# Kernel tuning notes

Hardware: AMD Instinct MI355X
Metric: run time of the kernel (lower is better)

The kernel has to match this reference:

```python
import jax, jax.numpy as jnp
import numpy as np

B, S, D = 2, 2048, 768
H = 12
HD = D // H


def setup_inputs() -> dict:
    key = jax.random.key(0)
    ks = jax.random.split(key, 9)
    s_in = 1.0 / np.sqrt(D)
    return {
        "x": jax.random.normal(ks[0], (B, S, D), dtype=jnp.float32),
        "wq": jax.random.normal(ks[1], (D, D), dtype=jnp.float32) * s_in,
        "bq": jax.random.normal(ks[2], (D,), dtype=jnp.float32) * 0.01,
        "wk": jax.random.normal(ks[3], (D, D), dtype=jnp.float32) * s_in,
        "bk": jax.random.normal(ks[4], (D,), dtype=jnp.float32) * 0.01,
        "wv": jax.random.normal(ks[5], (D, D), dtype=jnp.float32) * s_in,
        "bv": jax.random.normal(ks[6], (D,), dtype=jnp.float32) * 0.01,
        "wo": jax.random.normal(ks[7], (D, D), dtype=jnp.float32) * s_in,
        "bo": jax.random.normal(ks[8], (D,), dtype=jnp.float32) * 0.01,
    }


def reference(x, wq, bq, wk, bk, wv, bv, wo, bo):
    b, s, _ = x.shape
    # projections -> [b, h, s, hd]
    def proj(w, bias):
        return (x @ w + bias).reshape(b, s, H, HD).transpose(0, 2, 1, 3)
    q = proj(wq, bq)
    k = proj(wk, bk)
    v = proj(wv, bv)
    scores = jnp.einsum("bhqd,bhkd->bhqk", q, k)
    causal = jnp.triu(jnp.ones((s, s), dtype=bool), k=1)
    scores = jnp.where(causal, -jnp.inf, scores)
    attn = jax.nn.softmax(scores / np.sqrt(HD), axis=-1)
    # dropout p=0.0 -> identity
    ctx = jnp.einsum("bhqk,bhkd->bhqd", attn, v)
    ctx = ctx.transpose(0, 2, 1, 3).reshape(b, s, D)
    return ctx @ wo + bo
```

## Files before the change

kernel.cpp:

```cpp
#include <hip/hip_runtime.h>
#include <math.h>

#define BB  2
#define SS  2048
#define DD  768
#define HH  12
#define HDD 64
#define BSR (BB * SS)
#define NQT (SS / 64)
#define NCH 80
#define NKT 12

typedef __attribute__((ext_vector_type(8))) short bf16x8;
typedef __attribute__((ext_vector_type(4))) float f32x4;
typedef __attribute__((ext_vector_type(4))) int  i32x4;

__device__ inline f32x4 mfma16(bf16x8 a, bf16x8 b, f32x4 c) {
    return __builtin_amdgcn_mfma_f32_16x16x32_bf16(a, b, c, 0, 0, 0);
}

__device__ inline unsigned short f2b(float f) {
    unsigned int u = __float_as_uint(f);
    u += 0x7FFFu + ((u >> 16) & 1u);
    return (unsigned short)(u >> 16);
}
__device__ inline float b2f(unsigned short u) {
    return __uint_as_float((unsigned int)u << 16);
}

__device__ inline unsigned int cvt_pk_bf16(float lo, float hi) {
    unsigned int r;
    asm("v_cvt_pk_bf16_f32 %0, %1, %2" : "=v"(r) : "v"(lo), "v"(hi));
    return r;
}

__device__ inline void async_copy16(void* lds, const void* g) {
    __builtin_amdgcn_global_load_lds(
        (const __attribute__((address_space(1))) unsigned int*)g,
        (__attribute__((address_space(3))) unsigned int*)lds, 16, 0, 0);
}

__global__ __launch_bounds__(256) void conv_wT_kernel(
    const float* __restrict__ w0, const float* __restrict__ w1,
    const float* __restrict__ w2, const float* __restrict__ w3,
    unsigned short* __restrict__ o0, unsigned short* __restrict__ o1,
    unsigned short* __restrict__ o2, unsigned short* __restrict__ o3)
{
    const float* w = (blockIdx.z == 0) ? w0 : (blockIdx.z == 1) ? w1
                   : (blockIdx.z == 2) ? w2 : w3;
    unsigned short* o = (blockIdx.z == 0) ? o0 : (blockIdx.z == 1) ? o1
                      : (blockIdx.z == 2) ? o2 : o3;
    const int n0 = blockIdx.x * 64;
    const int k0 = blockIdx.y * 64;
    const int tid = threadIdx.x;

    __shared__ unsigned short tile[64][72];

#pragma unroll
    for (int p = 0; p < 4; ++p) {
        int c  = p * 256 + tid;
        int kr = c >> 4;
        int nc = (c & 15) * 4;
        float4 v = *(const float4*)&w[(size_t)(k0 + kr) * DD + n0 + nc];
        tile[nc + 0][kr] = f2b(v.x);
        tile[nc + 1][kr] = f2b(v.y);
        tile[nc + 2][kr] = f2b(v.z);
        tile[nc + 3][kr] = f2b(v.w);
    }
    __syncthreads();
#pragma unroll
    for (int p = 0; p < 2; ++p) {
        int c  = p * 256 + tid;
        int nr = c >> 3;
        int kc = (c & 7) * 8;
        *(i32x4*)&o[(size_t)(n0 + nr) * DD + k0 + kc] = *(const i32x4*)&tile[nr][kc];
    }
}

__global__ __launch_bounds__(256) void qkv_gemm_kernel(
    const float* __restrict__ x,
    const unsigned short* __restrict__ wqT, const unsigned short* __restrict__ wkT,
    const unsigned short* __restrict__ wvT,
    const float* __restrict__ bq, const float* __restrict__ bk,
    const float* __restrict__ bv,
    unsigned short* __restrict__ Qg, unsigned short* __restrict__ Kg,
    unsigned short* __restrict__ Vg)
{
    const int which = blockIdx.z;
    const unsigned short* Bt = (which == 0) ? wqT : (which == 1) ? wkT : wvT;
    const float* bias        = (which == 0) ? bq  : (which == 1) ? bk  : bv;
    unsigned short* out      = (which == 0) ? Qg  : (which == 1) ? Kg  : Vg;
    const float qs           = (which == 0) ? 0.18033688011112042f : 1.0f;

    const int m0 = blockIdx.x * 64;
    const int n0 = blockIdx.y * 128;
    const int tid  = threadIdx.x;
    const int w    = tid >> 6;
    const int lane = tid & 63;
    const int quad = lane >> 4;
    const int l16  = lane & 15;
    const int mh   = w & 1;
    const int nh   = w >> 1;
    const int swz  = l16 & 7;

    __shared__ unsigned short smem[24576];
    unsigned short (*As0)[64] = (unsigned short(*)[64])smem;
    unsigned short (*Bs0)[64] = (unsigned short(*)[64])(smem + 4096);
    unsigned short (*As1)[64] = (unsigned short(*)[64])(smem + 12288);
    unsigned short (*Bs1)[64] = (unsigned short(*)[64])(smem + 16384);
    unsigned short (*T)[136]  = (unsigned short(*)[136])smem;

    const int rA0 = tid >> 3,          jA0 = tid & 7,          chA0 = jA0 ^ (rA0 & 7);
    const int rA1 = (256 + tid) >> 3,  jA1 = tid & 7,          chA1 = jA1 ^ (rA1 & 7);
    const float* xr0 = &x[(size_t)(m0 + rA0) * DD + chA0 * 8];
    const float* xr1 = &x[(size_t)(m0 + rA1) * DD + chA1 * 8];
    int ldsA0 = rA0 * 64 + jA0 * 8;
    int ldsA1 = rA1 * 64 + jA1 * 8;

    const unsigned short* gB[4];
    int ldsB[4];
#pragma unroll
    for (int p = 0; p < 4; ++p) {
        int c  = p * 256 + tid;
        int r  = c >> 3;
        int j  = c & 7;
        int ch = j ^ (r & 7);
        gB[p]   = &Bt[(size_t)(n0 + r) * DD + ch * 8];
        ldsB[p] = r * 64 + j * 8;
    }

    f32x4 zero = {0.f, 0.f, 0.f, 0.f};
    f32x4 acc[2][4];
#pragma unroll
    for (int i = 0; i < 2; ++i)
#pragma unroll
        for (int j = 0; j < 4; ++j) acc[i][j] = zero;

    {
        float4 pf0 = *(const float4*)(xr0);
        float4 pf1 = *(const float4*)(xr0 + 4);
        float4 pf2 = *(const float4*)(xr1);
        float4 pf3 = *(const float4*)(xr1 + 4);
#pragma unroll
        for (int p = 0; p < 4; ++p)
            async_copy16((unsigned short*)Bs0 + ldsB[p], gB[p]);
        i32x4 tv;
        tv[0] = (int)cvt_pk_bf16(pf0.x, pf0.y);
        tv[1] = (int)cvt_pk_bf16(pf0.z, pf0.w);
        tv[2] = (int)cvt_pk_bf16(pf1.x, pf1.y);
        tv[3] = (int)cvt_pk_bf16(pf1.z, pf1.w);
        *(i32x4*)((unsigned short*)As0 + ldsA0) = tv;
        tv[0] = (int)cvt_pk_bf16(pf2.x, pf2.y);
        tv[1] = (int)cvt_pk_bf16(pf2.z, pf2.w);
        tv[2] = (int)cvt_pk_bf16(pf3.x, pf3.y);
        tv[3] = (int)cvt_pk_bf16(pf3.z, pf3.w);
        *(i32x4*)((unsigned short*)As1 + 0) = tv;
        *(i32x4*)((unsigned short*)As0 + ldsA1) = tv;
    }
    __syncthreads();

#pragma unroll
    for (int t = 0; t < NKT; ++t) {
        const int kn = (t + 1) * 64;
        unsigned short (*As)[64] = (t & 1) ? As1 : As0;
        unsigned short (*Bs)[64] = (t & 1) ? Bs1 : Bs0;
        unsigned short (*An)[64] = (t & 1) ? As0 : As1;
        unsigned short (*Bn)[64] = (t & 1) ? Bs0 : Bs1;
        const bool more = (t + 1 < NKT);

        float4 pf0, pf1, pf2, pf3;
        if (more) {
            pf0 = *(const float4*)(xr0 + kn);
            pf1 = *(const float4*)(xr0 + kn + 4);
            pf2 = *(const float4*)(xr1 + kn);
            pf3 = *(const float4*)(xr1 + kn + 4);
#pragma unroll
            for (int p = 0; p < 4; ++p)
                async_copy16((unsigned short*)Bn + ldsB[p], gB[p] + kn);
        }

        bf16x8 af0[2], af1[2], bf0[4], bf1[4];
#pragma unroll
        for (int mt = 0; mt < 2; ++mt) {
            int r = mh * 32 + mt * 16 + l16;
            af0[mt] = *(const bf16x8*)&As[r][((quad    ) ^ swz) * 8];
            af1[mt] = *(const bf16x8*)&As[r][((quad + 4) ^ swz) * 8];
        }
#pragma unroll
        for (int nt = 0; nt < 4; ++nt) {
            int r = nh * 64 + nt * 16 + l16;
            bf0[nt] = *(const bf16x8*)&Bs[r][((quad    ) ^ swz) * 8];
            bf1[nt] = *(const bf16x8*)&Bs[r][((quad + 4) ^ swz) * 8];
        }
#pragma unroll
        for (int mt = 0; mt < 2; ++mt)
#pragma unroll
            for (int nt = 0; nt < 4; ++nt) {
                acc[mt][nt] = mfma16(af0[mt], bf0[nt], acc[mt][nt]);
                acc[mt][nt] = mfma16(af1[mt], bf1[nt], acc[mt][nt]);
            }

        if (more) {
            i32x4 tv;
            tv[0] = (int)cvt_pk_bf16(pf0.x, pf0.y);
            tv[1] = (int)cvt_pk_bf16(pf0.z, pf0.w);
            tv[2] = (int)cvt_pk_bf16(pf1.x, pf1.y);
            tv[3] = (int)cvt_pk_bf16(pf1.z, pf1.w);
            *(i32x4*)((unsigned short*)An + ldsA0) = tv;
            tv[0] = (int)cvt_pk_bf16(pf2.x, pf2.y);
            tv[1] = (int)cvt_pk_bf16(pf2.z, pf2.w);
            tv[2] = (int)cvt_pk_bf16(pf3.x, pf3.y);
            tv[3] = (int)cvt_pk_bf16(pf3.z, pf3.w);
            *(i32x4*)((unsigned short*)An + ldsA1) = tv;
        }
        __syncthreads();
    }

    if (which < 2) {
#pragma unroll
        for (int nt = 0; nt < 4; ++nt) {
            const int col = nh * 64 + nt * 16 + l16;
            const float bvv = bias[n0 + col];
#pragma unroll
            for (int mt = 0; mt < 2; ++mt)
#pragma unroll
                for (int r = 0; r < 4; ++r)
                    T[mh * 32 + mt * 16 + quad * 4 + r][col] =
                        f2b((acc[mt][nt][r] + bvv) * qs);
        }
        __syncthreads();
#pragma unroll
        for (int p2 = 0; p2 < 4; ++p2) {
            int c    = p2 * 256 + tid;
            int row  = c >> 4;
            int ck   = c & 15;
            int head = ck >> 3;
            int wi   = ck & 7;
            int sg   = m0 + row;
            int bi   = sg >> 11, si = sg & 2047;
            int hcol = (n0 >> 6) + head;
            *(i32x4*)&out[(((size_t)(bi * HH + hcol)) * SS + si) * HDD + wi * 8] =
                *(const i32x4*)&T[row][head * 64 + wi * 8];
        }
    } else {
        for (int pass = 0; pass < 2; ++pass) {
            if (pass) __syncthreads();
            if (nh == pass) {
#pragma unroll
                for (int nt = 0; nt < 4; ++nt) {
                    const float bvv = bias[n0 + pass * 64 + nt * 16 + l16];
#pragma unroll
                    for (int mt = 0; mt < 2; ++mt) {
                        uint2 pk;
                        pk.x = cvt_pk_bf16(acc[mt][nt][0] + bvv, acc[mt][nt][1] + bvv);
                        pk.y = cvt_pk_bf16(acc[mt][nt][2] + bvv, acc[mt][nt][3] + bvv);
                        *(uint2*)&T[nt * 16 + l16][mh * 32 + mt * 16 + quad * 4] = pk;
                    }
                }
            }
            __syncthreads();
            const int bi   = m0 >> 11;
            const int s0   = m0 & 2047;
            const int hcol = (n0 >> 6) + pass;
#pragma unroll
            for (int p2 = 0; p2 < 2; ++p2) {
                int c    = p2 * 256 + tid;
                int drow = c >> 3;
                int wi   = c & 7;
                *(i32x4*)&out[(((size_t)(bi * HH + hcol)) * HDD + drow) * SS + s0 + wi * 8] =
                    *(const i32x4*)&T[drow][wi * 8];
            }
        }
    }
}

__global__ __launch_bounds__(256) void out_gemm_kernel(
    const unsigned short* __restrict__ cb, const unsigned short* __restrict__ woT,
    const float* __restrict__ bo, float* __restrict__ out)
{
    const int m0 = blockIdx.x * 64;
    const int n0 = blockIdx.y * 128;
    const int tid  = threadIdx.x;
    const int w    = tid >> 6;
    const int lane = tid & 63;
    const int quad = lane >> 4;
    const int l16  = lane & 15;
    const int mh   = w & 1;
    const int nh   = w >> 1;
    const int swz  = l16 & 7;

    __shared__ unsigned short smem[24576];
    unsigned short (*As0)[64] = (unsigned short(*)[64])smem;
    unsigned short (*Bs0)[64] = (unsigned short(*)[64])(smem + 4096);
    unsigned short (*As1)[64] = (unsigned short(*)[64])(smem + 12288);
    unsigned short (*Bs1)[64] = (unsigned short(*)[64])(smem + 16384);

    const unsigned short* gA[2];
    int ldsA[2];
#pragma unroll
    for (int p = 0; p < 2; ++p) {
        int c  = p * 256 + tid;
        int r  = c >> 3;
        int j  = c & 7;
        int ch = j ^ (r & 7);
        gA[p]   = &cb[(size_t)(m0 + r) * DD + ch * 8];
        ldsA[p] = r * 64 + j * 8;
    }
    const unsigned short* gB[4];
    int ldsB[4];
#pragma unroll
    for (int p = 0; p < 4; ++p) {
        int c  = p * 256 + tid;
        int r  = c >> 3;
        int j  = c & 7;
        int ch = j ^ (r & 7);
        gB[p]   = &woT[(size_t)(n0 + r) * DD + ch * 8];
        ldsB[p] = r * 64 + j * 8;
    }

    f32x4 zero = {0.f, 0.f, 0.f, 0.f};
    f32x4 acc[2][4];
#pragma unroll
    for (int i = 0; i < 2; ++i)
#pragma unroll
        for (int j = 0; j < 4; ++j) acc[i][j] = zero;

#pragma unroll
    for (int p = 0; p < 2; ++p) async_copy16((unsigned short*)As0 + ldsA[p], gA[p]);
#pragma unroll
    for (int p = 0; p < 4; ++p) async_copy16((unsigned short*)Bs0 + ldsB[p], gB[p]);
    __syncthreads();

#pragma unroll
    for (int t = 0; t < NKT; ++t) {
        const int kn = (t + 1) * 64;
        unsigned short (*As)[64] = (t & 1) ? As1 : As0;
        unsigned short (*Bs)[64] = (t & 1) ? Bs1 : Bs0;
        unsigned short (*An)[64] = (t & 1) ? As0 : As1;
        unsigned short (*Bn)[64] = (t & 1) ? Bs0 : Bs1;
        if (t + 1 < NKT) {
#pragma unroll
            for (int p = 0; p < 2; ++p)
                async_copy16((unsigned short*)An + ldsA[p], gA[p] + kn);
#pragma unroll
            for (int p = 0; p < 4; ++p)
                async_copy16((unsigned short*)Bn + ldsB[p], gB[p] + kn);
        }
        bf16x8 af0[2], af1[2], bf0[4], bf1[4];
#pragma unroll
        for (int mt = 0; mt < 2; ++mt) {
            int r = mh * 32 + mt * 16 + l16;
            af0[mt] = *(const bf16x8*)&As[r][((quad    ) ^ swz) * 8];
            af1[mt] = *(const bf16x8*)&As[r][((quad + 4) ^ swz) * 8];
        }
#pragma unroll
        for (int nt = 0; nt < 4; ++nt) {
            int r = nh * 64 + nt * 16 + l16;
            bf0[nt] = *(const bf16x8*)&Bs[r][((quad    ) ^ swz) * 8];
            bf1[nt] = *(const bf16x8*)&Bs[r][((quad + 4) ^ swz) * 8];
        }
#pragma unroll
        for (int mt = 0; mt < 2; ++mt)
#pragma unroll
            for (int nt = 0; nt < 4; ++nt) {
                acc[mt][nt] = mfma16(af0[mt], bf0[nt], acc[mt][nt]);
                acc[mt][nt] = mfma16(af1[mt], bf1[nt], acc[mt][nt]);
            }
        __syncthreads();
    }

#pragma unroll
    for (int nt = 0; nt < 4; ++nt) {
        const int n = n0 + nh * 64 + nt * 16 + l16;
        const float bvv = bo[n];
#pragma unroll
        for (int mt = 0; mt < 2; ++mt) {
            const int mbase = m0 + mh * 32 + mt * 16 + quad * 4;
#pragma unroll
            for (int r = 0; r < 4; ++r)
                out[(size_t)(mbase + r) * DD + n] = acc[mt][nt][r] + bvv;
        }
    }
}

__global__ __launch_bounds__(256, 4) void attn_mfma_kernel(
    const unsigned short* __restrict__ Qg, const unsigned short* __restrict__ Kg,
    const unsigned short* __restrict__ Vg, unsigned short* __restrict__ Opart,
    float* __restrict__ Lb)
{
    const int c = (NCH - 1) - blockIdx.x;
    int qt, ck;
    if (c < 8)       { qt = c;                             ck = 0;     }
    else if (c < 24) { int t = c - 8;  qt = 8  + (t >> 1); ck = t & 1; }
    else if (c < 48) { int t = c - 24; qt = 16 + t / 3;    ck = t % 3; }
    else             { int t = c - 48; qt = 24 + (t >> 2); ck = t & 3; }
    const int lo = ck * 8;
    const int hi = min(lo + 8, qt + 1);

    const int h  = blockIdx.y;
    const int b  = blockIdx.z;
    const int tid  = threadIdx.x;
    const int w    = tid >> 6;
    const int lane = tid & 63;
    const int quad = lane >> 4;
    const int l16  = lane & 15;
    const int q0   = qt * 64;

    const size_t bh = (size_t)(b * HH + h);
    const unsigned short* qp = Qg + bh * SS * HDD;
    const unsigned short* kp = Kg + bh * SS * HDD;
    const unsigned short* vp = Vg + bh * HDD * SS;

    unsigned short* op = Opart + ((size_t)bh * NCH + c) * 64 * HDD;
    float* lp = Lb + ((size_t)bh * NCH + c) * 64;

    const int qlocal = w * 16 + l16;
    const int query  = q0 + qlocal;

    __shared__ unsigned short Ks[64][64];
    __shared__ unsigned short Vt[64][64];
    __shared__ unsigned short PsT[4][16][72];
    unsigned short* slab = &PsT[w][0][0];

    const bf16x8 qb0 = *(const bf16x8*)&qp[(size_t)query * HDD + quad * 8];
    const bf16x8 qb1 = *(const bf16x8*)&qp[(size_t)query * HDD + 32 + quad * 8];

    const int pr  = tid >> 3;
    const int po8 = tid & 7;
    const int fs  = l16 & 7;

    i32x4 kpre[2], vpre[2];
#pragma unroll
    for (int p = 0; p < 2; ++p) {
        int r  = pr + p * 32;
        int gc = (po8 ^ (r & 7)) * 8;
        kpre[p] = *(const i32x4*)&kp[(size_t)(lo * 64 + r) * HDD + gc];
        vpre[p] = *(const i32x4*)&vp[(size_t)r * SS + lo * 64 + gc];
    }

    f32x4 zero = {0.f, 0.f, 0.f, 0.f};
    f32x4 o_acc[4];
    float l_i = 0.f;
#pragma unroll
    for (int i = 0; i < 4; ++i) o_acc[i] = zero;

    for (int kt = lo; kt < hi; ++kt) {
        const int k0 = kt * 64;
        __syncthreads();
#pragma unroll
        for (int p = 0; p < 2; ++p) {
            int r = pr + p * 32;
            *(i32x4*)&Ks[r][po8 * 8] = kpre[p];
            *(i32x4*)&Vt[r][po8 * 8] = vpre[p];
        }
        __syncthreads();

        if (kt + 1 < hi) {
            const int kn = (kt + 1) * 64;
#pragma unroll
            for (int p = 0; p < 2; ++p) {
                int r  = pr + p * 32;
                int gc = (po8 ^ (r & 7)) * 8;
                kpre[p] = *(const i32x4*)&kp[(size_t)(kn + r) * HDD + gc];
                vpre[p] = *(const i32x4*)&vp[(size_t)r * SS + kn + gc];
            }
        }

        f32x4 s_acc[4];
#pragma unroll
        for (int t = 0; t < 4; ++t) {
            const int row = t * 16 + l16;
            bf16x8 klo = *(const bf16x8*)&Ks[row][((quad    ) ^ fs) * 8];
            bf16x8 khi = *(const bf16x8*)&Ks[row][((quad + 4) ^ fs) * 8];
            s_acc[t] = mfma16(klo, qb0, zero);
            s_acc[t] = mfma16(khi, qb1, s_acc[t]);
        }

        float ps[4][4];
#pragma unroll
        for (int t = 0; t < 4; ++t)
#pragma unroll
            for (int r = 0; r < 4; ++r) {
                const int key = k0 + t * 16 + quad * 4 + r;
                float pv = exp2f(s_acc[t][r]);
                if (kt == qt && key > query) pv = 0.f;
                ps[t][r] = pv;
                l_i += pv;
            }

#pragma unroll
        for (int t = 0; t < 4; ++t) {
            uint2 pk;
            pk.x = cvt_pk_bf16(ps[t][0], ps[t][1]);
            pk.y = cvt_pk_bf16(ps[t][2], ps[t][3]);
            *(uint2*)&slab[l16 * 72 + t * 16 + quad * 4] = pk;
        }
        bf16x8 pb0 = *(const bf16x8*)&slab[l16 * 72 + quad * 8];
        bf16x8 pb1 = *(const bf16x8*)&slab[l16 * 72 + 32 + quad * 8];

#pragma unroll
        for (int t2 = 0; t2 < 4; ++t2) {
            const int row = t2 * 16 + l16;
            bf16x8 vlo = *(const bf16x8*)&Vt[row][((quad    ) ^ fs) * 8];
            bf16x8 vhi = *(const bf16x8*)&Vt[row][((quad + 4) ^ fs) * 8];
            o_acc[t2] = mfma16(vlo, pb0, o_acc[t2]);
            o_acc[t2] = mfma16(vhi, pb1, o_acc[t2]);
        }
    }

    l_i += __shfl_xor(l_i, 16);
    l_i += __shfl_xor(l_i, 32);
    if (quad == 0) lp[qlocal] = l_i;
#pragma unroll
    for (int t2 = 0; t2 < 4; ++t2) {
        uint2 pk;
        pk.x = cvt_pk_bf16(o_acc[t2][0], o_acc[t2][1]);
        pk.y = cvt_pk_bf16(o_acc[t2][2], o_acc[t2][3]);
        *(uint2*)&slab[l16 * 72 + t2 * 16 + quad * 4] = pk;
    }
#pragma unroll
    for (int p2 = 0; p2 < 2; ++p2) {
        int cc  = p2 * 64 + lane;
        int row = cc >> 3, dc = cc & 7;
        *(i32x4*)&op[(size_t)(w * 16 + row) * HDD + dc * 8] =
            *(const i32x4*)&slab[row * 72 + dc * 8];
    }
}

__global__ __launch_bounds__(256) void merge_kernel(
    const unsigned short* __restrict__ Opart, const float* __restrict__ Lb,
    unsigned short* __restrict__ cb)
{
    const int qt  = blockIdx.x;
    const int bhn = blockIdx.y;
    const int b   = bhn / HH, h = bhn % HH;
    const int tid = threadIdx.x;
    const int row = tid >> 2;
    const int d0  = (tid & 3) * 16;
    const int q   = qt * 64 + row;

    const int nch = (qt < 8) ? 1 : (qt < 16) ? 2 : (qt < 24) ? 3 : 4;
    const int cb0 = (qt < 8) ? qt
                  : (qt < 16) ? (8  + (qt - 8)  * 2)
                  : (qt < 24) ? (24 + (qt - 16) * 3)
                  :             (48 + (qt - 24) * 4);

    float suml = 0.f;
    float accv[16];
#pragma unroll
    for (int i = 0; i < 16; ++i) accv[i] = 0.f;

    for (int ci = 0; ci < nch; ++ci) {
        const size_t base = (size_t)bhn * NCH + cb0 + ci;
        suml += Lb[base * 64 + row];
        const unsigned short* o = Opart + (base * 64 + row) * HDD + d0;
        i32x4 va = *(const i32x4*)&o[0];
        i32x4 vb = *(const i32x4*)&o[8];
#pragma unroll
        for (int wd = 0; wd < 4; ++wd) {
            unsigned int ua = (unsigned int)va[wd];
            accv[wd * 2 + 0] += __uint_as_float(ua << 16);
            accv[wd * 2 + 1] += __uint_as_float(ua & 0xffff0000u);
            unsigned int ub = (unsigned int)vb[wd];
            accv[8 + wd * 2 + 0] += __uint_as_float(ub << 16);
            accv[8 + wd * 2 + 1] += __uint_as_float(ub & 0xffff0000u);
        }
    }
    const float inv = 1.0f / suml;
    unsigned int res[8];
#pragma unroll
    for (int i = 0; i < 8; ++i)
        res[i] = cvt_pk_bf16(accv[2 * i] * inv, accv[2 * i + 1] * inv);
    unsigned short* dst = &cb[((size_t)(b * SS + q)) * DD + h * HDD + d0];
    *(i32x4*)&dst[0] = *(const i32x4*)&res[0];
    *(i32x4*)&dst[8] = *(const i32x4*)&res[4];
}

extern "C" void kernel_launch(void* const* d_in, const int* in_sizes, int n_in,
                              void* d_out, int out_size, void* d_ws, size_t ws_size,
                              hipStream_t stream)
{
    const float* x  = (const float*)d_in[0];
    const float* wq = (const float*)d_in[1];
    const float* bq = (const float*)d_in[2];
    const float* wk = (const float*)d_in[3];
    const float* bk = (const float*)d_in[4];
    const float* wv = (const float*)d_in[5];
    const float* bv = (const float*)d_in[6];
    const float* wo = (const float*)d_in[7];
    const float* bo = (const float*)d_in[8];
    float* out = (float*)d_out;

    char* p = (char*)d_ws;
    const size_t XB  = (size_t)BSR * DD * 2;
    const size_t WB  = (size_t)DD * DD * 2;
    const size_t OPB = (size_t)BB * HH * NCH * 64 * HDD * 2;
    const size_t LBB = (size_t)BB * HH * NCH * 64 * 4;
    unsigned short* wqT = (unsigned short*)p;            p += WB;
    unsigned short* wkT = (unsigned short*)p;            p += WB;
    unsigned short* wvT = (unsigned short*)p;            p += WB;
    unsigned short* woT = (unsigned short*)p;            p += WB;
    unsigned short* Qg  = (unsigned short*)p;            p += XB;
    unsigned short* Kg  = (unsigned short*)p;            p += XB;
    unsigned short* Vg  = (unsigned short*)p;            p += XB;
    unsigned short* cb  = (unsigned short*)p;            p += XB;
    unsigned short* Opart = (unsigned short*)p;          p += OPB;
    float* Lb = (float*)p;                               p += LBB;

    conv_wT_kernel<<<dim3(DD / 64, DD / 64, 4), 256, 0, stream>>>(
        wq, wk, wv, wo, wqT, wkT, wvT, woT);
    qkv_gemm_kernel<<<dim3(BSR / 64, DD / 128, 3), 256, 0, stream>>>(
        x, wqT, wkT, wvT, bq, bk, bv, Qg, Kg, Vg);
    attn_mfma_kernel<<<dim3(NCH, HH, BB), 256, 0, stream>>>(
        Qg, Kg, Vg, Opart, Lb);
    merge_kernel<<<dim3(NQT, BB * HH), 256, 0, stream>>>(Opart, Lb, cb);
    out_gemm_kernel<<<dim3(BSR / 64, DD / 128), 256, 0, stream>>>(cb, woT, bo, out);
}
```

Measured before the change: 161.2 us.

## Process 128 queries per attention block with two query fragments per wave

```diff
diff --git a/kernel.cpp b/kernel.cpp
--- a/kernel.cpp
+++ b/kernel.cpp
@@ -7,8 +7,7 @@
 #define HH  12
 #define HDD 64
 #define BSR (BB * SS)
-#define NQT (SS / 64)
-#define NCH 80
+#define NCH 40
 #define NKT 12
 
 typedef __attribute__((ext_vector_type(8))) short bf16x8;
@@ -154,7 +153,6 @@
         tv[1] = (int)cvt_pk_bf16(pf2.z, pf2.w);
         tv[2] = (int)cvt_pk_bf16(pf3.x, pf3.y);
         tv[3] = (int)cvt_pk_bf16(pf3.z, pf3.w);
-        *(i32x4*)((unsigned short*)As1 + 0) = tv;
         *(i32x4*)((unsigned short*)As0 + ldsA1) = tv;
     }
     __syncthreads();
@@ -389,13 +387,16 @@
     float* __restrict__ Lb)
 {
     const int c = (NCH - 1) - blockIdx.x;
-    int qt, ck;
-    if (c < 8)       { qt = c;                             ck = 0;     }
-    else if (c < 24) { int t = c - 8;  qt = 8  + (t >> 1); ck = t & 1; }
-    else if (c < 48) { int t = c - 24; qt = 16 + t / 3;    ck = t % 3; }
-    else             { int t = c - 48; qt = 24 + (t >> 2); ck = t & 3; }
-    const int lo = ck * 8;
-    const int hi = min(lo + 8, qt + 1);
+    int qt, ck, nch;
+    if (c < 4)       { qt = c;                            ck = 0;     nch = 1; }
+    else if (c < 12) { int t = c - 4;  qt = 4  + (t >> 1); ck = t & 1; nch = 2; }
+    else if (c < 24) { int t = c - 12; qt = 8  + t / 3;    ck = t % 3; nch = 3; }
+    else             { int t = c - 24; qt = 12 + (t >> 2); ck = t & 3; nch = 4; }
+    const int NT   = 2 * qt + 2;
+    const int base = NT / nch, rem = NT % nch;
+    const int lo   = ck * base + min(ck, rem);
+    const int hi   = lo + base + (ck < rem ? 1 : 0);
+    const int dlo  = 2 * qt;
 
     const int h  = blockIdx.y;
     const int b  = blockIdx.z;
@@ -404,26 +405,29 @@
     const int lane = tid & 63;
     const int quad = lane >> 4;
     const int l16  = lane & 15;
-    const int q0   = qt * 64;
+    const int q0   = qt * 128;
 
     const size_t bh = (size_t)(b * HH + h);
     const unsigned short* qp = Qg + bh * SS * HDD;
     const unsigned short* kp = Kg + bh * SS * HDD;
     const unsigned short* vp = Vg + bh * HDD * SS;
 
-    unsigned short* op = Opart + ((size_t)bh * NCH + c) * 64 * HDD;
-    float* lp = Lb + ((size_t)bh * NCH + c) * 64;
-
-    const int qlocal = w * 16 + l16;
-    const int query  = q0 + qlocal;
+    unsigned short* op = Opart + ((size_t)bh * NCH + c) * 128 * HDD;
+    float* lp = Lb + ((size_t)bh * NCH + c) * 128;
 
     __shared__ unsigned short Ks[64][64];
     __shared__ unsigned short Vt[64][64];
-    __shared__ unsigned short PsT[4][16][72];
-    unsigned short* slab = &PsT[w][0][0];
-
-    const bf16x8 qb0 = *(const bf16x8*)&qp[(size_t)query * HDD + quad * 8];
-    const bf16x8 qb1 = *(const bf16x8*)&qp[(size_t)query * HDD + 32 + quad * 8];
+    __shared__ unsigned short PsT[4][2][16][72];
+    unsigned short* slab = &PsT[w][0][0][0];
+
+    bf16x8 qb0[2], qb1[2];
+    int query[2];
+#pragma unroll
+    for (int qf = 0; qf < 2; ++qf) {
+        query[qf] = q0 + w * 32 + qf * 16 + l16;
+        qb0[qf] = *(const bf16x8*)&qp[(size_t)query[qf] * HDD + quad * 8];
+        qb1[qf] = *(const bf16x8*)&qp[(size_t)query[qf] * HDD + 32 + quad * 8];
+    }
 
     const int pr  = tid >> 3;
     const int po8 = tid & 7;
@@ -439,10 +443,12 @@
     }
 
     f32x4 zero = {0.f, 0.f, 0.f, 0.f};
-    f32x4 o_acc[4];
-    float l_i = 0.f;
-#pragma unroll
-    for (int i = 0; i < 4; ++i) o_acc[i] = zero;
+    f32x4 o_acc[2][4];
+    float l_i[2] = {0.f, 0.f};
+#pragma unroll
+    for (int qf = 0; qf < 2; ++qf)
+#pragma unroll
+        for (int i = 0; i < 4; ++i) o_acc[qf][i] = zero;
 
     for (int kt = lo; kt < hi; ++kt) {
         const int k0 = kt * 64;
@@ -466,63 +472,70 @@
             }
         }
 
-        f32x4 s_acc[4];
+        const bool diag = (kt >= dlo);
 #pragma unroll
         for (int t = 0; t < 4; ++t) {
             const int row = t * 16 + l16;
             bf16x8 klo = *(const bf16x8*)&Ks[row][((quad    ) ^ fs) * 8];
             bf16x8 khi = *(const bf16x8*)&Ks[row][((quad + 4) ^ fs) * 8];
-            s_acc[t] = mfma16(klo, qb0, zero);
-            s_acc[t] = mfma16(khi, qb1, s_acc[t]);
-        }
-
-        float ps[4][4];
-#pragma unroll
-        for (int t = 0; t < 4; ++t)
-#pragma unroll
-            for (int r = 0; r < 4; ++r) {
-                const int key = k0 + t * 16 + quad * 4 + r;
-                float pv = exp2f(s_acc[t][r]);
-                if (kt == qt && key > query) pv = 0.f;
-                ps[t][r] = pv;
-                l_i += pv;
+#pragma unroll
+            for (int qf = 0; qf < 2; ++qf) {
+                f32x4 s = mfma16(klo, qb0[qf], zero);
+                s = mfma16(khi, qb1[qf], s);
+                float pv[4];
+#pragma unroll
+                for (int r = 0; r < 4; ++r) {
+                    const int key = k0 + t * 16 + quad * 4 + r;
+                    float p = exp2f(s[r]);
+                    if (diag && key > query[qf]) p = 0.f;
+                    pv[r] = p;
+                    l_i[qf] += p;
+                }
+                uint2 pk;
+                pk.x = cvt_pk_bf16(pv[0], pv[1]);
+                pk.y = cvt_pk_bf16(pv[2], pv[3]);
+                *(uint2*)&slab[(qf * 16 + l16) * 72 + t * 16 + quad * 4] = pk;
             }
-
-#pragma unroll
-        for (int t = 0; t < 4; ++t) {
-            uint2 pk;
-            pk.x = cvt_pk_bf16(ps[t][0], ps[t][1]);
-            pk.y = cvt_pk_bf16(ps[t][2], ps[t][3]);
-            *(uint2*)&slab[l16 * 72 + t * 16 + quad * 4] = pk;
-        }
-        bf16x8 pb0 = *(const bf16x8*)&slab[l16 * 72 + quad * 8];
-        bf16x8 pb1 = *(const bf16x8*)&slab[l16 * 72 + 32 + quad * 8];
-
+        }
+
+        bf16x8 pb0[2], pb1[2];
+#pragma unroll
+        for (int qf = 0; qf < 2; ++qf) {
+            pb0[qf] = *(const bf16x8*)&slab[(qf * 16 + l16) * 72 + quad * 8];
+            pb1[qf] = *(const bf16x8*)&slab[(qf * 16 + l16) * 72 + 32 + quad * 8];
+        }
 #pragma unroll
         for (int t2 = 0; t2 < 4; ++t2) {
             const int row = t2 * 16 + l16;
             bf16x8 vlo = *(const bf16x8*)&Vt[row][((quad    ) ^ fs) * 8];
             bf16x8 vhi = *(const bf16x8*)&Vt[row][((quad + 4) ^ fs) * 8];
-            o_acc[t2] = mfma16(vlo, pb0, o_acc[t2]);
-            o_acc[t2] = mfma16(vhi, pb1, o_acc[t2]);
-        }
-    }
-
-    l_i += __shfl_xor(l_i, 16);
-    l_i += __shfl_xor(l_i, 32);
-    if (quad == 0) lp[qlocal] = l_i;
-#pragma unroll
-    for (int t2 = 0; t2 < 4; ++t2) {
-        uint2 pk;
-        pk.x = cvt_pk_bf16(o_acc[t2][0], o_acc[t2][1]);
-        pk.y = cvt_pk_bf16(o_acc[t2][2], o_acc[t2][3]);
-        *(uint2*)&slab[l16 * 72 + t2 * 16 + quad * 4] = pk;
-    }
-#pragma unroll
-    for (int p2 = 0; p2 < 2; ++p2) {
+#pragma unroll
+            for (int qf = 0; qf < 2; ++qf) {
+                o_acc[qf][t2] = mfma16(vlo, pb0[qf], o_acc[qf][t2]);
+                o_acc[qf][t2] = mfma16(vhi, pb1[qf], o_acc[qf][t2]);
+            }
+        }
+    }
+
+#pragma unroll
+    for (int qf = 0; qf < 2; ++qf) {
+        float l = l_i[qf];
+        l += __shfl_xor(l, 16);
+        l += __shfl_xor(l, 32);
+        if (quad == 0) lp[w * 32 + qf * 16 + l16] = l;
+#pragma unroll
+        for (int t2 = 0; t2 < 4; ++t2) {
+            uint2 pk;
+            pk.x = cvt_pk_bf16(o_acc[qf][t2][0], o_acc[qf][t2][1]);
+            pk.y = cvt_pk_bf16(o_acc[qf][t2][2], o_acc[qf][t2][3]);
+            *(uint2*)&slab[(qf * 16 + l16) * 72 + t2 * 16 + quad * 4] = pk;
+        }
+    }
+#pragma unroll
+    for (int p2 = 0; p2 < 4; ++p2) {
         int cc  = p2 * 64 + lane;
         int row = cc >> 3, dc = cc & 7;
-        *(i32x4*)&op[(size_t)(w * 16 + row) * HDD + dc * 8] =
+        *(i32x4*)&op[(size_t)(w * 32 + row) * HDD + dc * 8] =
             *(const i32x4*)&slab[row * 72 + dc * 8];
     }
 }
@@ -531,19 +544,22 @@
     const unsigned short* __restrict__ Opart, const float* __restrict__ Lb,
     unsigned short* __restrict__ cb)
 {
-    const int qt  = blockIdx.x;
-    const int bhn = blockIdx.y;
-    const int b   = bhn / HH, h = bhn % HH;
-    const int tid = threadIdx.x;
-    const int row = tid >> 2;
-    const int d0  = (tid & 3) * 16;
-    const int q   = qt * 64 + row;
-
-    const int nch = (qt < 8) ? 1 : (qt < 16) ? 2 : (qt < 24) ? 3 : 4;
-    const int cb0 = (qt < 8) ? qt
-                  : (qt < 16) ? (8  + (qt - 8)  * 2)
-                  : (qt < 24) ? (24 + (qt - 16) * 3)
-                  :             (48 + (qt - 24) * 4);
+    const int bx   = blockIdx.x;
+    const int qt2  = bx >> 1;
+    const int half = bx & 1;
+    const int bhn  = blockIdx.y;
+    const int b    = bhn / HH, h = bhn % HH;
+    const int tid  = threadIdx.x;
+    const int row  = tid >> 2;
+    const int d0   = (tid & 3) * 16;
+    const int rowc = half * 64 + row;
+    const int q    = qt2 * 128 + rowc;
+
+    const int nch = (qt2 < 4) ? 1 : (qt2 < 8) ? 2 : (qt2 < 12) ? 3 : 4;
+    const int cb0 = (qt2 < 4) ? qt2
+                  : (qt2 < 8)  ? (4  + (qt2 - 4)  * 2)
+                  : (qt2 < 12) ? (12 + (qt2 - 8)  * 3)
+                  :              (24 + (qt2 - 12) * 4);
 
     float suml = 0.f;
     float accv[16];
@@ -552,8 +568,8 @@
 
     for (int ci = 0; ci < nch; ++ci) {
         const size_t base = (size_t)bhn * NCH + cb0 + ci;
-        suml += Lb[base * 64 + row];
-        const unsigned short* o = Opart + (base * 64 + row) * HDD + d0;
+        suml += Lb[base * 128 + rowc];
+        const unsigned short* o = Opart + (base * 128 + rowc) * HDD + d0;
         i32x4 va = *(const i32x4*)&o[0];
         i32x4 vb = *(const i32x4*)&o[8];
 #pragma unroll
@@ -594,8 +610,8 @@
     char* p = (char*)d_ws;
     const size_t XB  = (size_t)BSR * DD * 2;
     const size_t WB  = (size_t)DD * DD * 2;
-    const size_t OPB = (size_t)BB * HH * NCH * 64 * HDD * 2;
-    const size_t LBB = (size_t)BB * HH * NCH * 64 * 4;
+    const size_t OPB = (size_t)BB * HH * NCH * 128 * HDD * 2;
+    const size_t LBB = (size_t)BB * HH * NCH * 128 * 4;
     unsigned short* wqT = (unsigned short*)p;            p += WB;
     unsigned short* wkT = (unsigned short*)p;            p += WB;
     unsigned short* wvT = (unsigned short*)p;            p += WB;
@@ -613,6 +629,6 @@
         x, wqT, wkT, wvT, bq, bk, bv, Qg, Kg, Vg);
     attn_mfma_kernel<<<dim3(NCH, HH, BB), 256, 0, stream>>>(
         Qg, Kg, Vg, Opart, Lb);
-    merge_kernel<<<dim3(NQT, BB * HH), 256, 0, stream>>>(Opart, Lb, cb);
+    merge_kernel<<<dim3(32, BB * HH), 256, 0, stream>>>(Opart, Lb, cb);
     out_gemm_kernel<<<dim3(BSR / 64, DD / 128), 256, 0, stream>>>(cb, woT, bo, out);
 }
```

Result: no change. 162.9 us (+1.1%).
